# Kernel optimization log

Measured on AMD Instinct MI355X. Metric: run time of the kernel, lower is better.

## Reference

```python
import jax, jax.numpy as jnp
import numpy as np

PAD = 3            # pad_size
K = 3              # kernel_size
MAX_DISP = 20      # max_displacement
STRIDE1 = 1
STRIDE2 = 2

B, C, H, W = 4, 128, 192, 192


def _correlation(input1, input2):
    """FlowNetC/PWC-Net correlation cost volume (correlation_pwc semantics).

    input1, input2: [B, C, H, W]
    returns: [B, D*D, Hout, Wout] where D = 2*(MAX_DISP//STRIDE2)+1.
    """
    b, c, h, w = input1.shape
    kr = (K - 1) // 2                      # kernel radius
    br = kr + MAX_DISP                     # border radius
    hp, wp = h + 2 * PAD, w + 2 * PAD      # padded sizes
    hout = (hp - 2 * br) // STRIDE1
    wout = (wp - 2 * br) // STRIDE1
    gr = MAX_DISP // STRIDE2               # neighborhood grid radius
    disp = jnp.arange(-gr, gr + 1, dtype=jnp.int32) * STRIDE2
    # channel order: tj (dy) outer, ti (dx) inner, matching the CUDA kernel
    dyx = jnp.stack(jnp.meshgrid(disp, disp, indexing='ij'), axis=-1).reshape(-1, 2)

    pad1 = jnp.pad(input1, ((0, 0), (0, 0), (PAD, PAD), (PAD, PAD)))
    pad2 = jnp.pad(input2, ((0, 0), (0, 0), (PAD, PAD), (PAD, PAD)))

    # region of pad1 touched by all outputs (stride1 == 1)
    hh, ww = hout * STRIDE1 + 2 * kr, wout * STRIDE1 + 2 * kr
    s1 = pad1[:, :, MAX_DISP:MAX_DISP + hh, MAX_DISP:MAX_DISP + ww]
    nelems = K * K * c

    def step(_, d):
        dy, dx = d[0], d[1]
        s2 = jax.lax.dynamic_slice(pad2, (0, 0, MAX_DISP + dy, MAX_DISP + dx),
                                   (b, c, hh, ww))
        prod = jnp.sum(s1 * s2, axis=1)  # [B, hh, ww] reduce channels
        summed = jax.lax.reduce_window(prod, 0.0, jax.lax.add,
                                       (1, K, K), (1, STRIDE1, STRIDE1), 'VALID')
        return None, summed / nelems      # [B, Hout, Wout]

    _, out = jax.lax.scan(step, None, dyx)   # [D*D, B, Hout, Wout]
    return jnp.transpose(out, (1, 0, 2, 3))  # [B, D*D, Hout, Wout]


def setup_inputs() -> dict:
    key = jax.random.key(0)
    k1, k2 = jax.random.split(key)
    input1 = jax.random.normal(k1, (B, C, H, W), dtype=jnp.float32)
    input2 = jax.random.normal(k2, (B, C, H, W), dtype=jnp.float32)
    return {"input1": input1, "input2": input2}


def reference(input1, input2):
    return _correlation(input1, input2)
```

## Files before the change

kernel.cpp:

```cpp
#include <hip/hip_runtime.h>
#include <hip/hip_bf16.h>


#define C_    128
#define H_    192
#define W_    192
#define HW_   36864
#define NE_   18874368
#define CORR_E 44036496
#define WS_NEED 163570464ull

typedef __attribute__((ext_vector_type(8))) short short8;
typedef __attribute__((ext_vector_type(4))) float floatx4;

__device__ __forceinline__ float bf2f(ushort h) {
    uint u = ((uint)h) << 16;
    return __builtin_bit_cast(float, u);
}
__device__ __forceinline__ ushort f2bf(float f) {
    __hip_bfloat16 hb = __float2bfloat16(f);
    return *(ushort*)&hb;
}

__global__ __launch_bounds__(256)
void cvt_t_kernel(const float* __restrict__ a, const float* __restrict__ b,
                  ushort* __restrict__ dst0) {
    __shared__ float tile[128 * 65];
    const float* src = blockIdx.z ? b : a;
    ushort* dst = dst0 + (size_t)blockIdx.z * NE_;
    const int bb = blockIdx.y;
    const int hw0 = blockIdx.x * 64;
    const int t = threadIdx.x;
    const int xr = (t & 15) * 4;
    const int c0 = t >> 4;
    const float* sbase = src + (size_t)bb * C_ * HW_ + hw0;
#pragma unroll
    for (int pass = 0; pass < 8; ++pass) {
        const int c = c0 + 16 * pass;
        float4 v = *(const float4*)(sbase + (size_t)c * HW_ + xr);
        float* lp = &tile[c * 65 + xr];
        lp[0] = v.x; lp[1] = v.y; lp[2] = v.z; lp[3] = v.w;
    }
    __syncthreads();
    ushort* obase = dst + ((size_t)bb * HW_ + hw0) * 128;
#pragma unroll
    for (int pass = 0; pass < 4; ++pass) {
        const int u = t + 256 * pass;
        const int x = u >> 4, oc = u & 15;
        uint w[4];
#pragma unroll
        for (int k = 0; k < 4; ++k) {
            const float f0 = tile[(oc * 8 + 2 * k) * 65 + x];
            const float f1 = tile[(oc * 8 + 2 * k + 1) * 65 + x];
            w[k] = (uint)f2bf(f0) | ((uint)f2bf(f1) << 16);
        }
        uint4 o; o.x = w[0]; o.y = w[1]; o.z = w[2]; o.w = w[3];
        *(uint4*)(obase + (size_t)x * 128 + oc * 8) = o;
    }
}

__global__ __launch_bounds__(256, 4)
void corr_mfma(const ushort* __restrict__ in1t, const ushort* __restrict__ in2t,
               ushort* __restrict__ corrw) {
    __shared__ ushort ctile[2][21 * 136];
    const int tid = threadIdx.x;
    const int lin = blockIdx.x + 5 * (blockIdx.y + 20 * blockIdx.z);
    const int zz = lin & 7;
    const int rem = lin >> 3;
    const int j0 = (rem % 5) * 32;
    const int ytile = rem / 5;
    const int b = zz >> 1, q = zz & 1;
    const int ybase = q + 8 * ytile;
    const int lane = tid & 63, wav = tid >> 6;
    const int yrow = wav >> 1, p = wav & 1;
    const int mn = lane & 15, quad = lane >> 4;

    const int ax = j0 + 17 + 2 * mn + p;
    short8 afr[2][4];
#pragma unroll
    for (int a = 0; a < 2; ++a) {
        const int arow = ybase + 2 * yrow + 4 * a + 17;
        const ushort* aptr = in1t + ((size_t)((b * H_ + arow) * W_ + ax)) * C_ + quad * 8;
#pragma unroll
        for (int kb = 0; kb < 4; ++kb) afr[a][kb] = *(const short8*)(aptr + kb * 32);
    }

    const int ybY = ybase + 2 * yrow - 3;
    const ushort* bptr[3];
    bool colok[3];
#pragma unroll
    for (int u3 = 0; u3 < 3; ++u3) {
        const int s = u3 * 16 + mn;
        const int xp = j0 - 3 + p + 2 * s;
        colok[u3] = ((unsigned)xp < (unsigned)W_) && (s <= 36);
        bptr[u3] = in2t + (ptrdiff_t)((b * H_ + ybY) * W_ + xp) * C_ + quad * 8;
    }

    const short8 z8 = {0, 0, 0, 0, 0, 0, 0, 0};
    const size_t planebase = (size_t)b * 441;

    for (int dyi = 0; dyi < 21; ++dyi) {
        floatx4 acc[2][3];
#pragma unroll
        for (int a = 0; a < 2; ++a)
#pragma unroll
            for (int u3 = 0; u3 < 3; ++u3) acc[a][u3] = (floatx4){0.f, 0.f, 0.f, 0.f};
#pragma unroll
        for (int a = 0; a < 2; ++a) {
            const int yb = ybY + 2 * dyi + 4 * a;
            if ((unsigned)yb < (unsigned)H_) {
                const ptrdiff_t roff = (ptrdiff_t)(2 * dyi + 4 * a) * W_ * C_;
#pragma unroll
                for (int u3 = 0; u3 < 3; ++u3) {
                    short8 b0 = z8, b1 = z8, b2 = z8, b3 = z8;
                    if (colok[u3]) {
                        const ushort* bp = bptr[u3] + roff;
                        b0 = *(const short8*)(bp);
                        b1 = *(const short8*)(bp + 32);
                        b2 = *(const short8*)(bp + 64);
                        b3 = *(const short8*)(bp + 96);
                    }
                    acc[a][u3] = __builtin_amdgcn_mfma_f32_16x16x32_bf16(afr[a][0], b0, acc[a][u3], 0, 0, 0);
                    acc[a][u3] = __builtin_amdgcn_mfma_f32_16x16x32_bf16(afr[a][1], b1, acc[a][u3], 0, 0, 0);
                    acc[a][u3] = __builtin_amdgcn_mfma_f32_16x16x32_bf16(afr[a][2], b2, acc[a][u3], 0, 0, 0);
                    acc[a][u3] = __builtin_amdgcn_mfma_f32_16x16x32_bf16(afr[a][3], b3, acc[a][u3], 0, 0, 0);
                }
            }
        }

        ushort* ct = &ctile[dyi & 1][0];
#pragma unroll
        for (int a = 0; a < 2; ++a) {
            const int rr = yrow + 2 * a;
#pragma unroll
            for (int u3 = 0; u3 < 3; ++u3) {
#pragma unroll
                for (int v = 0; v < 4; ++v) {
                    const int mr = quad * 4 + v;
                    const int t = u3 * 16 + mn - mr;
                    if (t >= 0 && t <= 20)
                        ct[t * 136 + rr * 34 + 2 * mr + p] = f2bf(acc[a][u3][v]);
                }
            }
        }
        __syncthreads();
#pragma unroll
        for (int it = 0; it < 6; ++it) {
            const int idx = tid + it * 256;
            if (idx < 1344) {
                const int t = idx >> 6, rem2 = idx & 63;
                const int rr = rem2 >> 4, x2 = (rem2 & 15) << 1;
                const uint val = *(const uint*)(ct + t * 136 + rr * 34 + x2);
                const int Y = ybase + 2 * rr, X = j0 + x2;
                if (Y < 158 && X < 158) {
                    const size_t off = ((planebase + (size_t)(dyi * 21 + t)) * 158 + Y) * 158 + X;
                    *(uint*)(corrw + off) = val;
                }
            }
        }
    }
}

__global__ __launch_bounds__(256)
void window_kernel(const ushort* __restrict__ corrw, float* __restrict__ out) {
    __shared__ uint wsl[1440];
    const int tid = threadIdx.x;
    const int i0 = blockIdx.x * 16;
    const int plane = blockIdx.y;
    const ushort* cp = corrw + (size_t)plane * 24964;
    for (int task = tid; task < 1440; task += 256) {
        const int r = task / 80;
        const int dc = task - r * 80;
        const int row = i0 + r;
        if (dc < 79 && row < 158)
            wsl[task] = *(const uint*)(cp + row * 158 + dc * 2);
    }
    __syncthreads();
    if (tid < 156) {
        const ushort* cl = (const ushort*)wsl;
        float S[18];
#pragma unroll
        for (int r = 0; r < 18; ++r) {
            const ushort* rp = cl + r * 160 + tid;
            S[r] = bf2f(rp[0]) + bf2f(rp[1]) + bf2f(rp[2]);
        }
        const float sc = 1.f / 1152.f;
#pragma unroll
        for (int r = 0; r < 16; ++r) {
            const int row = i0 + r;
            if (row < 156)
                out[(size_t)plane * 24336 + (size_t)row * 156 + tid] =
                    (S[r] + S[r + 1] + S[r + 2]) * sc;
        }
    }
}

#define OUT_HW 156
#define NDISP 21
#define TILE_OUT 14
#define TILE_CORR 16
#define S2W 56
#define NT 256

__global__ __launch_bounds__(NT, 4)
void corr_fallback(const float* __restrict__ in1, const float* __restrict__ in2,
                   float* __restrict__ out) {
    __shared__ float s2s[TILE_CORR * S2W];
    __shared__ float corrs[NDISP * TILE_CORR * TILE_CORR];
    const int tid = threadIdx.x;
    const int tx = tid & 15;
    const int ty = tid >> 4;
    const int tj = blockIdx.x;
    const int ti = blockIdx.y;
    const int z = blockIdx.z;
    const int b = z / NDISP;
    const int dyi = z - b * NDISP;
    const int dy = 2 * dyi - 20;
    const int y0 = ti * TILE_OUT;
    const int x0 = tj * TILE_OUT;
    const int y = y0 + ty;
    const int x = x0 + tx;
    float acc[NDISP];
#pragma unroll
    for (int d = 0; d < NDISP; ++d) acc[d] = 0.f;
    const float* p1 = in1 + (size_t)b * C_ * HW_ + (size_t)(y + 17) * W_ + (x + 17);
    const float* p2base = in2 + (size_t)b * C_ * HW_;
    for (int c = 0; c < C_; ++c) {
        const float a = p1[(size_t)c * HW_];
        const float* p2 = p2base + (size_t)c * HW_;
        for (int idx = tid; idx < TILE_CORR * S2W; idx += NT) {
            const int r = idx / S2W;
            const int cc = idx - r * S2W;
            const int gr = y0 + r + 17 + dy;
            const int gc = x0 + cc - 3;
            float v = 0.f;
            if ((unsigned)gr < H_ && (unsigned)gc < W_) v = p2[gr * W_ + gc];
            s2s[idx] = v;
        }
        __syncthreads();
        const float* srow = &s2s[ty * S2W + tx];
#pragma unroll
        for (int d = 0; d < NDISP; ++d) acc[d] += a * srow[2 * d];
        __syncthreads();
    }
#pragma unroll
    for (int d = 0; d < NDISP; ++d)
        corrs[d * (TILE_CORR * TILE_CORR) + tid] = acc[d];
    __syncthreads();
    const float scale = 1.f / 1152.f;
    for (int o = tid; o < NDISP * TILE_OUT * TILE_OUT; o += NT) {
        const int d = o / (TILE_OUT * TILE_OUT);
        const int rem = o - d * (TILE_OUT * TILE_OUT);
        const int i = rem / TILE_OUT;
        const int j = rem - i * TILE_OUT;
        const float* cpt = &corrs[d * (TILE_CORR * TILE_CORR) + i * TILE_CORR + j];
        const float s = cpt[0] + cpt[1] + cpt[2]
                      + cpt[16] + cpt[17] + cpt[18]
                      + cpt[32] + cpt[33] + cpt[34];
        const int ig = y0 + i;
        const int jg = x0 + j;
        if (ig < OUT_HW && jg < OUT_HW) {
            const size_t oidx = (((size_t)b * (NDISP * NDISP) + (size_t)dyi * NDISP + d)
                                 * OUT_HW + ig) * OUT_HW + jg;
            out[oidx] = s * scale;
        }
    }
}

extern "C" void kernel_launch(void* const* d_in, const int* in_sizes, int n_in,
                              void* d_out, int out_size, void* d_ws, size_t ws_size,
                              hipStream_t stream) {
    const float* in1 = (const float*)d_in[0];
    const float* in2 = (const float*)d_in[1];
    float* out = (float*)d_out;

    if (ws_size >= WS_NEED) {
        ushort* wsp = (ushort*)d_ws;
        ushort* in1t = wsp;
        ushort* in2t = wsp + (size_t)NE_;
        ushort* corrw = wsp + (size_t)2 * NE_;
        cvt_t_kernel<<<dim3(576, 4, 2), 256, 0, stream>>>(in1, in2, wsp);
        corr_mfma<<<dim3(5, 20, 8), 256, 0, stream>>>(in1t, in2t, corrw);
        window_kernel<<<dim3(10, 1764), 256, 0, stream>>>(corrw, out);
    } else {
        corr_fallback<<<dim3(12, 12, 84), 256, 0, stream>>>(in1, in2, out);
    }
}
```

Measured before the change: 506.6 us.

## Split corr displacement rows across blocks, convert-then-transpose in LDS, taller window tiles

The correlation kernel now splits the 21 vertical displacements into three chunks of 7 across a tripled grid. This raises block count and occupancy (launch bound 6) at the cost of reloading the A fragments three times. The transpose kernel converts to bf16 before storing to LDS, halving shared memory and allowing 16-byte vector reads on the output side. The window kernel processes 32 output rows per block with a rolling 3-row sum, reducing halo reloads and register use.

Measured after the change: 616.4 us. +21.7%, slower.

```diff
diff --git a/kernel.cpp b/kernel.cpp
--- a/kernel.cpp
+++ b/kernel.cpp
@@ -25,7 +25,7 @@
 __global__ __launch_bounds__(256)
 void cvt_t_kernel(const float* __restrict__ a, const float* __restrict__ b,
                   ushort* __restrict__ dst0) {
-    __shared__ float tile[128 * 65];
+    __shared__ ushort tile[64 * 132];
     const float* src = blockIdx.z ? b : a;
     ushort* dst = dst0 + (size_t)blockIdx.z * NE_;
     const int bb = blockIdx.y;
@@ -38,8 +38,10 @@
     for (int pass = 0; pass < 8; ++pass) {
         const int c = c0 + 16 * pass;
         float4 v = *(const float4*)(sbase + (size_t)c * HW_ + xr);
-        float* lp = &tile[c * 65 + xr];
-        lp[0] = v.x; lp[1] = v.y; lp[2] = v.z; lp[3] = v.w;
+        tile[(xr + 0) * 132 + c] = f2bf(v.x);
+        tile[(xr + 1) * 132 + c] = f2bf(v.y);
+        tile[(xr + 2) * 132 + c] = f2bf(v.z);
+        tile[(xr + 3) * 132 + c] = f2bf(v.w);
     }
     __syncthreads();
     ushort* obase = dst + ((size_t)bb * HW_ + hw0) * 128;
@@ -47,19 +49,12 @@
     for (int pass = 0; pass < 4; ++pass) {
         const int u = t + 256 * pass;
         const int x = u >> 4, oc = u & 15;
-        uint w[4];
-#pragma unroll
-        for (int k = 0; k < 4; ++k) {
-            const float f0 = tile[(oc * 8 + 2 * k) * 65 + x];
-            const float f1 = tile[(oc * 8 + 2 * k + 1) * 65 + x];
-            w[k] = (uint)f2bf(f0) | ((uint)f2bf(f1) << 16);
-        }
-        uint4 o; o.x = w[0]; o.y = w[1]; o.z = w[2]; o.w = w[3];
-        *(uint4*)(obase + (size_t)x * 128 + oc * 8) = o;
-    }
-}
-
-__global__ __launch_bounds__(256, 4)
+        short8 vv = *(const short8*)&tile[x * 132 + oc * 8];
+        *(short8*)(obase + (size_t)x * 128 + oc * 8) = vv;
+    }
+}
+
+__global__ __launch_bounds__(256, 6)
 void corr_mfma(const ushort* __restrict__ in1t, const ushort* __restrict__ in2t,
                ushort* __restrict__ corrw) {
     __shared__ ushort ctile[2][21 * 136];
@@ -68,7 +63,9 @@
     const int zz = lin & 7;
     const int rem = lin >> 3;
     const int j0 = (rem % 5) * 32;
-    const int ytile = rem / 5;
+    const int r2 = rem / 5;
+    const int ytile = r2 % 20;
+    const int d0 = (r2 / 20) * 7;
     const int b = zz >> 1, q = zz & 1;
     const int ybase = q + 8 * ytile;
     const int lane = tid & 63, wav = tid >> 6;
@@ -99,7 +96,7 @@
     const short8 z8 = {0, 0, 0, 0, 0, 0, 0, 0};
     const size_t planebase = (size_t)b * 441;
 
-    for (int dyi = 0; dyi < 21; ++dyi) {
+    for (int dyi = d0; dyi < d0 + 7; ++dyi) {
         floatx4 acc[2][3];
 #pragma unroll
         for (int a = 0; a < 2; ++a)
@@ -161,14 +158,14 @@
     }
 }
 
-__global__ __launch_bounds__(256)
+__global__ __launch_bounds__(192)
 void window_kernel(const ushort* __restrict__ corrw, float* __restrict__ out) {
-    __shared__ uint wsl[1440];
+    __shared__ uint wsl[34 * 80];
     const int tid = threadIdx.x;
-    const int i0 = blockIdx.x * 16;
+    const int i0 = blockIdx.x * 32;
     const int plane = blockIdx.y;
     const ushort* cp = corrw + (size_t)plane * 24964;
-    for (int task = tid; task < 1440; task += 256) {
+    for (int task = tid; task < 2720; task += 192) {
         const int r = task / 80;
         const int dc = task - r * 80;
         const int row = i0 + r;
@@ -178,19 +175,20 @@
     __syncthreads();
     if (tid < 156) {
         const ushort* cl = (const ushort*)wsl;
-        float S[18];
-#pragma unroll
-        for (int r = 0; r < 18; ++r) {
+        const float sc = 1.f / 1152.f;
+        const ushort* rp0 = cl + tid;
+        float s0 = bf2f(rp0[0]) + bf2f(rp0[1]) + bf2f(rp0[2]);
+        const ushort* rp1 = cl + 160 + tid;
+        float s1 = bf2f(rp1[0]) + bf2f(rp1[1]) + bf2f(rp1[2]);
+#pragma unroll
+        for (int r = 2; r < 34; ++r) {
             const ushort* rp = cl + r * 160 + tid;
-            S[r] = bf2f(rp[0]) + bf2f(rp[1]) + bf2f(rp[2]);
-        }
-        const float sc = 1.f / 1152.f;
-#pragma unroll
-        for (int r = 0; r < 16; ++r) {
-            const int row = i0 + r;
+            const float s2 = bf2f(rp[0]) + bf2f(rp[1]) + bf2f(rp[2]);
+            const int row = i0 + r - 2;
             if (row < 156)
                 out[(size_t)plane * 24336 + (size_t)row * 156 + tid] =
-                    (S[r] + S[r + 1] + S[r + 2]) * sc;
+                    (s0 + s1 + s2) * sc;
+            s0 = s1; s1 = s2;
         }
     }
 }
@@ -280,8 +278,8 @@
         ushort* in2t = wsp + (size_t)NE_;
         ushort* corrw = wsp + (size_t)2 * NE_;
         cvt_t_kernel<<<dim3(576, 4, 2), 256, 0, stream>>>(in1, in2, wsp);
-        corr_mfma<<<dim3(5, 20, 8), 256, 0, stream>>>(in1t, in2t, corrw);
-        window_kernel<<<dim3(10, 1764), 256, 0, stream>>>(corrw, out);
+        corr_mfma<<<dim3(5, 20, 24), 256, 0, stream>>>(in1t, in2t, corrw);
+        window_kernel<<<dim3(5, 1764), 192, 0, stream>>>(corrw, out);
     } else {
         corr_fallback<<<dim3(12, 12, 84), 256, 0, stream>>>(in1, in2, out);
     }
```
